# Optimization experiments

Measured on AMD Instinct MI355X. Metric: run time of the kernel, lower is better.

## Reference

```python
import jax, jax.numpy as jnp
import numpy as np

SEQ = 8192
DIM = 1280
NHEADS = 16
HEAD_DIM = DIM // NHEADS  # 80
NSEG = 8
SEG = SEQ // NSEG  # 1024


def setup_inputs() -> dict:
    key = jax.random.key(0)
    ks = jax.random.split(key, 7)
    hidden_states = jax.random.normal(ks[0], (SEQ, DIM), jnp.float32)
    # realistic rotary embeddings: cos/sin of random angles, shape [S, head_dim]
    ang = jax.random.uniform(ks[1], (SEQ, HEAD_DIM), jnp.float32, 0.0, 2.0 * np.pi)
    cos = jnp.cos(ang)
    sin = jnp.sin(ang)
    qkv_w = jax.random.normal(ks[2], (3 * DIM, DIM), jnp.float32) * (DIM ** -0.5)
    qkv_b = jax.random.normal(ks[3], (3 * DIM,), jnp.float32) * 0.02
    proj_w = jax.random.normal(ks[4], (DIM, DIM), jnp.float32) * (DIM ** -0.5)
    proj_b = jax.random.normal(ks[5], (DIM,), jnp.float32) * 0.02
    cu_seqlens = jnp.arange(NSEG + 1, dtype=jnp.int32) * SEG  # equal segments
    return {"hidden_states": hidden_states, "cos": cos, "sin": sin,
            "qkv_w": qkv_w, "qkv_b": qkv_b, "proj_w": proj_w, "proj_b": proj_b,
            "cu_seqlens": cu_seqlens}


def _rope(x, cos, sin):
    # x: [S, H, D]; cos/sin: [S, D] broadcast over heads. Computed in fp32.
    x = x.astype(jnp.float32)
    d = x.shape[-1]
    x1, x2 = x[..., : d // 2], x[..., d // 2:]
    rot = jnp.concatenate([-x2, x1], axis=-1)
    return x * cos[:, None, :] + rot * sin[:, None, :]


def reference(hidden_states, cos, sin, qkv_w, qkv_b, proj_w, proj_b, cu_seqlens):
    S, dim = hidden_states.shape
    nseg = cu_seqlens.shape[0] - 1
    seg = S // nseg  # segments are equal-length; block-diagonal attention batches over them
    H, D = NHEADS, dim // NHEADS

    qkv = hidden_states @ qkv_w.T + qkv_b                 # [S, 3*dim]
    qkv = qkv.reshape(S, 3, H, D)
    q, k, v = qkv[:, 0], qkv[:, 1], qkv[:, 2]             # [S, H, D]

    in_dtype = hidden_states.dtype
    q = _rope(q, cos, sin).astype(in_dtype)
    k = _rope(k, cos, sin).astype(in_dtype)

    scale = D ** -0.5
    qs = q.reshape(nseg, seg, H, D)
    ks = k.reshape(nseg, seg, H, D)
    vs = v.reshape(nseg, seg, H, D)

    scores = jnp.einsum('bqhd,bkhd->bhqk', qs, ks) * scale  # [nseg, H, seg, seg]
    probs = jax.nn.softmax(scores, axis=-1)
    out = jnp.einsum('bhqk,bkhd->bqhd', probs, vs)          # [nseg, seg, H, D]
    out = out.reshape(S, H * D)
    return out @ proj_w.T + proj_b
```

## Files before the change

kernel.cpp:

```cpp
#include <hip/hip_runtime.h>

#define SEQ 8192
#define DIM 1280
#define NHEADS 16
#define HD 80
#define HDP 96
#define NSEG 8
#define SEG 1024
#define KVB 64
#define NSTEP (SEG / KVB)
#define PST 72

typedef float f32x4 __attribute__((ext_vector_type(4)));
typedef short bf16x8 __attribute__((ext_vector_type(8)));
typedef unsigned int u32;

__device__ __forceinline__ float fast_exp2(float x) {
  return __builtin_amdgcn_exp2f(x);
}

__device__ __forceinline__ short f2bf(float f) {
  unsigned int u = __builtin_bit_cast(unsigned int, f);
  u = (u + 0x7fff + ((u >> 16) & 1)) >> 16;
  return (short)u;
}

__device__ __forceinline__ float bf2f(short s) {
  u32 u = ((u32)(unsigned short)s) << 16;
  return __builtin_bit_cast(float, u);
}

__device__ __forceinline__ u32 cvt_pk_bf16(float lo, float hi) {
  u32 r;
  asm("v_cvt_pk_bf16_f32 %0, %1, %2" : "=v"(r) : "v"(lo), "v"(hi));
  return r;
}

typedef __attribute__((address_space(1))) const unsigned int glds_src_t;
typedef __attribute__((address_space(3))) unsigned int glds_dst_t;
__device__ __forceinline__ void gload_lds16(const void* g, void* l) {
  __builtin_amdgcn_global_load_lds((glds_src_t*)g, (glds_dst_t*)l, 16, 0, 0);
}

__global__ void cast_f32_bf16(const float* __restrict__ in, short* __restrict__ out, int n) {
  int n4 = n >> 2;
  for (int i = blockIdx.x * blockDim.x + threadIdx.x; i < n4; i += gridDim.x * blockDim.x) {
    float4 v = ((const float4*)in)[i];
    short4 o;
    o.x = f2bf(v.x); o.y = f2bf(v.y); o.z = f2bf(v.z); o.w = f2bf(v.w);
    ((short4*)out)[i] = o;
  }
}

__global__ __launch_bounds__(512, 1) void gemm256(
    const short* __restrict__ A, const short* __restrict__ B,
    const float* __restrict__ bias, float* __restrict__ C,
    short* __restrict__ Cb, int M, int N, int K) {
  __shared__ short As[2][16384];
  __shared__ short Bs[2][16384];
  int tid = threadIdx.x;
  int w = tid >> 6, l = tid & 63;
  int lrow = l & 15, lg = l >> 4;
  int wm = w >> 2, wn = w & 3;
  int bid = blockIdx.x;
  int cpx = gridDim.x >> 3;
  int lid = (bid & 7) * cpx + (bid >> 3);
  int ntx = N >> 8;
  int m0 = (lid / ntx) * 256, n0 = (lid % ntx) * 256;

  const short* Ablk = A + (size_t)m0 * K;
  const short* Bblk = B + (size_t)n0 * K;

  f32x4 acc[8][4] = {};

#define STG_HALF(LDSB, GBASE, HALF, K0)                                       \
  {                                                                           \
    _Pragma("unroll") for (int rr = 0; rr < 2; rr++) {                        \
      int sb = rr * 512 + w * 64;                                             \
      int ss2 = sb + l;                                                       \
      int rl = ss2 >> 3, cc = ss2 & 7;                                        \
      int sl = cc ^ (rl & 7);                                                 \
      const short* sp = (GBASE) + (size_t)((HALF)*128 + rl) * K + (K0) + sl * 8; \
      gload_lds16(sp, (char*)(LDSB) + (HALF)*16384 + sb * 16);                \
    }                                                                         \
  }
#define LDA(MH, KS)                                                           \
  _Pragma("unroll") for (int mt = 0; mt < 4; mt++) {                          \
    int rowa = wm * 128 + ((MH)*4 + mt) * 16 + lrow;                          \
    int pa_ = ((KS)*4 + lg) ^ (rowa & 7);                                     \
    a[mt] = *(const bf16x8*)&As[cur][rowa * 64 + pa_ * 8];                    \
  }
#define LDB(KS)                                                               \
  _Pragma("unroll") for (int nt = 0; nt < 4; nt++) {                          \
    int rowb = wn * 64 + nt * 16 + lrow;                                      \
    int pb_ = ((KS)*4 + lg) ^ (rowb & 7);                                     \
    b[nt] = *(const bf16x8*)&Bs[cur][rowb * 64 + pb_ * 8];                    \
  }
#define MFMA16(MH)                                                            \
  _Pragma("unroll") for (int mt = 0; mt < 4; mt++)                            \
      _Pragma("unroll") for (int nt = 0; nt < 4; nt++)                        \
          acc[(MH)*4 + mt][nt] = __builtin_amdgcn_mfma_f32_16x16x32_bf16(     \
              a[mt], b[nt], acc[(MH)*4 + mt][nt], 0, 0, 0);

  {
    short* Ad = &As[0][0];
    short* Bd = &Bs[0][0];
    STG_HALF(Ad, Ablk, 0, 0);
    STG_HALF(Ad, Ablk, 1, 0);
    STG_HALF(Bd, Bblk, 0, 0);
    STG_HALF(Bd, Bblk, 1, 0);
  }
  asm volatile("s_waitcnt vmcnt(0)" ::: "memory");
  __builtin_amdgcn_s_barrier();
  asm volatile("" ::: "memory");

  int NT = K >> 6;
  for (int t = 0; t < NT; ++t) {
    int cur = t & 1;
    if (t + 1 < NT) {
      short* Ad = &As[cur ^ 1][0];
      short* Bd = &Bs[cur ^ 1][0];
      int k1 = (t + 1) << 6;
      STG_HALF(Ad, Ablk, 0, k1);
      STG_HALF(Ad, Ablk, 1, k1);
      STG_HALF(Bd, Bblk, 0, k1);
      STG_HALF(Bd, Bblk, 1, k1);
      asm volatile("s_waitcnt vmcnt(8)" ::: "memory");
    } else {
      asm volatile("s_waitcnt vmcnt(0)" ::: "memory");
    }
    __builtin_amdgcn_s_barrier();
    asm volatile("" ::: "memory");
    {
      bf16x8 a[4], b[4];
      __builtin_amdgcn_s_setprio(1);
      LDA(0, 0); LDB(0); MFMA16(0);
      LDA(1, 0); MFMA16(1);
      LDA(0, 1); LDB(1); MFMA16(0);
      LDA(1, 1); MFMA16(1);
      __builtin_amdgcn_s_setprio(0);
    }
    __builtin_amdgcn_s_barrier();
    asm volatile("" ::: "memory");
  }

  if (Cb) {
    short* E = &As[0][0];
#pragma unroll
    for (int s = 0; s < 4; s++) {
      __syncthreads();
      if (wm == (s >> 1)) {
#pragma unroll
        for (int mi = 0; mi < 4; mi++) {
          int mt2 = (s & 1) * 4 + mi;
#pragma unroll
          for (int nt = 0; nt < 4; nt++) {
            int col = wn * 64 + nt * 16 + lrow;
            float bv = bias[n0 + col];
#pragma unroll
            for (int r = 0; r < 4; r++)
              E[(mi * 16 + lg * 4 + r) * 264 + col] = f2bf(acc[mt2][nt][r] + bv);
          }
        }
      }
      __syncthreads();
#pragma unroll
      for (int j = 0; j < 4; j++) {
        int c = j * 512 + tid;
        int row = c >> 5, ch = c & 31;
        *(uint4*)&Cb[(size_t)(m0 + s * 64 + row) * N + n0 + ch * 8] =
            *(const uint4*)&E[row * 264 + ch * 8];
      }
    }
  } else {
#pragma unroll
    for (int nt = 0; nt < 4; nt++) {
      int col = n0 + wn * 64 + nt * 16 + lrow;
      float bv = bias[col];
#pragma unroll
      for (int mt = 0; mt < 8; mt++) {
        int mrow = m0 + wm * 128 + mt * 16 + lg * 4;
#pragma unroll
        for (int r = 0; r < 4; r++)
          C[(size_t)(mrow + r) * N + col] = acc[mt][nt][r] + bv;
      }
    }
  }
#undef STG_HALF
#undef LDA
#undef LDB
#undef MFMA16
}

__global__ __launch_bounds__(256) void gemm_bt_bias(
    const short* __restrict__ A, const short* __restrict__ B,
    const float* __restrict__ bias, float* __restrict__ C,
    short* __restrict__ Cb, int M, int N, int K) {
  __shared__ short As[2][128 * 64];
  __shared__ short Bs[2][128 * 64];
  int tid = threadIdx.x;
  int w = tid >> 6, l = tid & 63;
  int lrow = l & 15, lg = l >> 4;
  int bid = blockIdx.x;
  int cpx = gridDim.x >> 3;
  int lid = (bid & 7) * cpx + (bid >> 3);
  int ntx = N >> 7;
  int m0 = (lid / ntx) * 128, n0 = (lid % ntx) * 128;
  int wm = w & 1, wn = w >> 1;

  f32x4 acc[4][4] = {};

  const char* Abase = (const char*)A + (size_t)m0 * K * 2;
  const char* Bbase = (const char*)B + (size_t)n0 * K * 2;

#define STAGE_G(BUF, K0)                                                       \
  {                                                                            \
    _Pragma("unroll") for (int j = 0; j < 4; j++) {                            \
      int c = j * 256 + tid;                                                   \
      int row = c >> 3;                                                        \
      int slc = (c & 7) ^ (row & 7);                                           \
      size_t goff = (size_t)row * K * 2 + (size_t)(K0) * 2 + slc * 16;         \
      int loff = (j * 256 + w * 64) * 16;                                      \
      gload_lds16(Abase + goff, (char*)&As[BUF][0] + loff);                    \
      gload_lds16(Bbase + goff, (char*)&Bs[BUF][0] + loff);                    \
    }                                                                          \
  }

  STAGE_G(0, 0);
  asm volatile("s_waitcnt vmcnt(0)" ::: "memory");
  __builtin_amdgcn_s_barrier();
  asm volatile("" ::: "memory");

  for (int k0 = 0; k0 < K; k0 += 64) {
    int cur = (k0 >> 6) & 1;
    if (k0 + 64 < K) {
      STAGE_G(cur ^ 1, k0 + 64);
      asm volatile("s_waitcnt vmcnt(8)" ::: "memory");
    } else {
      asm volatile("s_waitcnt vmcnt(0)" ::: "memory");
    }
    __builtin_amdgcn_s_barrier();
    asm volatile("" ::: "memory");
#pragma unroll
    for (int kk = 0; kk < 2; kk++) {
      bf16x8 a[4], b[4];
#pragma unroll
      for (int mt = 0; mt < 4; mt++) {
        int row = wm * 64 + mt * 16 + lrow;
        int p = (kk * 4 + lg) ^ (row & 7);
        a[mt] = *(const bf16x8*)&As[cur][row * 64 + p * 8];
      }
#pragma unroll
      for (int nt = 0; nt < 4; nt++) {
        int row = wn * 64 + nt * 16 + lrow;
        int p = (kk * 4 + lg) ^ (row & 7);
        b[nt] = *(const bf16x8*)&Bs[cur][row * 64 + p * 8];
      }
#pragma unroll
      for (int mt = 0; mt < 4; mt++)
#pragma unroll
        for (int nt = 0; nt < 4; nt++)
          acc[mt][nt] = __builtin_amdgcn_mfma_f32_16x16x32_bf16(a[mt], b[nt], acc[mt][nt], 0, 0, 0);
    }
    __builtin_amdgcn_s_barrier();
    asm volatile("" ::: "memory");
  }

#pragma unroll
  for (int nt = 0; nt < 4; nt++) {
    int col = n0 + wn * 64 + nt * 16 + lrow;
    float bv = bias[col];
#pragma unroll
    for (int mt = 0; mt < 4; mt++) {
      int mrow = m0 + wm * 64 + mt * 16 + lg * 4;
      if (Cb) {
#pragma unroll
        for (int r = 0; r < 4; r++)
          Cb[(size_t)(mrow + r) * N + col] = f2bf(acc[mt][nt][r] + bv);
      } else {
#pragma unroll
        for (int r = 0; r < 4; r++)
          C[(size_t)(mrow + r) * N + col] = acc[mt][nt][r] + bv;
      }
    }
  }
}

__global__ void rope_qk(const short* __restrict__ qkv, const float* __restrict__ cosb,
                        const float* __restrict__ sinb, short* __restrict__ qg,
                        short* __restrict__ kg) {
  int t = blockIdx.x * blockDim.x + threadIdx.x;
  if (t >= SEQ * NHEADS * 40) return;
  int d = t % 40;
  int h = (t / 40) & 15;
  int s = t / 640;
  const short* row = qkv + (size_t)s * (3 * DIM);
  float c0 = cosb[s * HD + d], c1 = cosb[s * HD + d + 40];
  float s0 = sinb[s * HD + d], s1 = sinb[s * HD + d + 40];
  float x1 = bf2f(row[h * HD + d]), x2 = bf2f(row[h * HD + d + 40]);
  float q0 = x1 * c0 - x2 * s0;
  float q1 = x2 * c1 + x1 * s1;
  float y1 = bf2f(row[DIM + h * HD + d]), y2 = bf2f(row[DIM + h * HD + d + 40]);
  float k0 = y1 * c0 - y2 * s0;
  float k1 = y2 * c1 + y1 * s1;
  const float sc = 0.11180339887498949f * 1.4426950408889634f;
  size_t base = ((size_t)h * SEQ + s) * HDP;
  qg[base + d] = f2bf(q0 * sc);
  qg[base + d + 40] = f2bf(q1 * sc);
  kg[base + d] = f2bf(k0);
  kg[base + d + 40] = f2bf(k1);
  if (d < 16) { qg[base + 80 + d] = 0; kg[base + 80 + d] = 0; }
}

__global__ void v_transpose(const short* __restrict__ qkv, short* __restrict__ vt) {
  __shared__ short T[16][72];
  int st = blockIdx.x, dt = blockIdx.y, h = blockIdx.z;
  int d0 = dt * 16, s0 = st * 64;
  int t = threadIdx.x;
  int dd = t & 15, ss = t >> 4;
#pragma unroll
  for (int j = 0; j < 4; j++) {
    int s = ss + j * 16;
    T[dd][s] = qkv[(size_t)(s0 + s) * (3 * DIM) + 2 * DIM + h * HD + d0 + dd];
  }
  __syncthreads();
  int s2 = t & 63, dr = t >> 6;
#pragma unroll
  for (int j = 0; j < 4; j++) {
    int d = dr + j * 4;
    vt[((size_t)(h * HD + d0 + d)) * SEQ + s0 + s2] = T[d][s2];
  }
}

__global__ __launch_bounds__(256, 2) void attn_kernel(
    const short* __restrict__ qg, const short* __restrict__ kg,
    const short* __restrict__ vt, short* __restrict__ out) {
  __shared__ short Ks[2][64 * 128];
  __shared__ short Pl[4][32 * PST];
  int bid = blockIdx.x;
  int b = bid & 7, h = (bid >> 3) & 15, qt = bid >> 7;
  int tid = threadIdx.x;
  int w = tid >> 6, l = tid & 63;
  int lrow = l & 15, lg = l >> 4;
  int qbase_s = b * SEG + qt * 128 + w * 32;

  const short* qh = qg + (size_t)h * SEQ * HDP;
  const short* kh = kg + (size_t)h * SEQ * HDP;
  const short* vh = vt + (size_t)h * HD * SEQ;

#define STAGE_K(BUF, KEY0N)                                                    \
  {                                                                            \
    _Pragma("unroll") for (int sr = 0; sr < 4; sr++) {                         \
      int sbase = sr * 256 + w * 64;                                           \
      int ss = sbase + l;                                                      \
      int skey = ss >> 4, sc = ss & 15;                                        \
      int slc = sc ^ (skey & 7);                                               \
      const short* ssrc =                                                      \
          kh + (size_t)((KEY0N) + skey) * HDP + (slc < 12 ? slc * 8 : 0);      \
      gload_lds16(ssrc, (char*)&Ks[BUF][0] + sbase * 16);                      \
    }                                                                          \
  }

  bf16x8 qf[2][3];
#pragma unroll
  for (int mt = 0; mt < 2; mt++)
#pragma unroll
    for (int ks = 0; ks < 3; ks++)
      qf[mt][ks] = *(const bf16x8*)&qh[(size_t)(qbase_s + mt * 16 + lrow) * HDP + ks * 32 + lg * 8];

  f32x4 o[2][5] = {};
  float m_st[2] = {-1e30f, -1e30f};
  float l_st[2] = {0.f, 0.f};

  short* Pw = &Pl[w][0];

  STAGE_K(0, b * SEG);
  __syncthreads();

  for (int i = 0; i < NSTEP; i++) {
    int cur = i & 1;
    int key0 = b * SEG + i * KVB;
    if (i + 1 < NSTEP) {
      STAGE_K(cur ^ 1, key0 + KVB);
    }

    f32x4 sv[2][4] = {};
    __builtin_amdgcn_s_setprio(1);
#pragma unroll
    for (int kt = 0; kt < 4; kt++) {
      bf16x8 kf[3];
      int key = kt * 16 + lrow;
#pragma unroll
      for (int ks = 0; ks < 3; ks++) {
        int p = (ks * 4 + lg) ^ (key & 7);
        kf[ks] = *(const bf16x8*)&Ks[cur][key * 128 + p * 8];
      }
#pragma unroll
      for (int mt = 0; mt < 2; mt++)
#pragma unroll
        for (int ks = 0; ks < 3; ks++)
          sv[mt][kt] = __builtin_amdgcn_mfma_f32_16x16x32_bf16(kf[ks], qf[mt][ks], sv[mt][kt], 0, 0, 0);
    }
    __builtin_amdgcn_s_setprio(0);

    bf16x8 vf[5][2];
#pragma unroll
    for (int nt = 0; nt < 5; nt++)
#pragma unroll
      for (int ks = 0; ks < 2; ks++)
        vf[nt][ks] = *(const bf16x8*)&vh[(size_t)(nt * 16 + lrow) * SEQ + key0 + ks * 32 + lg * 8];

    float cm[2];
#pragma unroll
    for (int mt = 0; mt < 2; mt++) {
      float a0 = fmaxf(fmaxf(sv[mt][0][0], sv[mt][0][1]), fmaxf(sv[mt][0][2], sv[mt][0][3]));
      float a1 = fmaxf(fmaxf(sv[mt][1][0], sv[mt][1][1]), fmaxf(sv[mt][1][2], sv[mt][1][3]));
      float a2 = fmaxf(fmaxf(sv[mt][2][0], sv[mt][2][1]), fmaxf(sv[mt][2][2], sv[mt][2][3]));
      float a3 = fmaxf(fmaxf(sv[mt][3][0], sv[mt][3][1]), fmaxf(sv[mt][3][2], sv[mt][3][3]));
      float c = fmaxf(fmaxf(a0, a1), fmaxf(a2, a3));
      c = fmaxf(c, __shfl_xor(c, 16));
      c = fmaxf(c, __shfl_xor(c, 32));
      cm[mt] = c;
    }
    if (__any((cm[0] > m_st[0] + 8.f) || (cm[1] > m_st[1] + 8.f))) {
#pragma unroll
      for (int mt = 0; mt < 2; mt++) {
        float mn = fmaxf(m_st[mt], cm[mt]);
        float c = fast_exp2(m_st[mt] - mn);
        m_st[mt] = mn;
        l_st[mt] *= c;
        float cr[4];
#pragma unroll
        for (int r = 0; r < 4; r++) cr[r] = __shfl(c, lg * 4 + r);
#pragma unroll
        for (int nt = 0; nt < 5; nt++)
#pragma unroll
          for (int r = 0; r < 4; r++) o[mt][nt][r] *= cr[r];
      }
    }
#pragma unroll
    for (int mt = 0; mt < 2; mt++) {
      float rs = 0.f;
#pragma unroll
      for (int kt = 0; kt < 4; kt++) {
#pragma unroll
        for (int r = 0; r < 4; r++) {
          sv[mt][kt][r] = fast_exp2(sv[mt][kt][r] - m_st[mt]);
          rs += sv[mt][kt][r];
        }
        uint2 pk;
        pk.x = cvt_pk_bf16(sv[mt][kt][0], sv[mt][kt][1]);
        pk.y = cvt_pk_bf16(sv[mt][kt][2], sv[mt][kt][3]);
        *(uint2*)&Pw[(mt * 16 + lrow) * PST + kt * 16 + lg * 4] = pk;
      }
      rs += __shfl_xor(rs, 16);
      rs += __shfl_xor(rs, 32);
      l_st[mt] += rs;
    }

    bf16x8 pa[2][2];
#pragma unroll
    for (int mt = 0; mt < 2; mt++)
#pragma unroll
      for (int ks = 0; ks < 2; ks++)
        pa[mt][ks] = *(const bf16x8*)&Pw[(mt * 16 + lrow) * PST + ks * 32 + lg * 8];
    __builtin_amdgcn_s_setprio(1);
#pragma unroll
    for (int nt = 0; nt < 5; nt++)
#pragma unroll
      for (int mt = 0; mt < 2; mt++)
#pragma unroll
        for (int ks = 0; ks < 2; ks++)
          o[mt][nt] = __builtin_amdgcn_mfma_f32_16x16x32_bf16(pa[mt][ks], vf[nt][ks], o[mt][nt], 0, 0, 0);
    __builtin_amdgcn_s_setprio(0);

    __syncthreads();
  }

#pragma unroll
  for (int mt = 0; mt < 2; mt++) {
    float rl = 1.f / l_st[mt];
    float ir[4];
#pragma unroll
    for (int r = 0; r < 4; r++) ir[r] = __shfl(rl, lg * 4 + r);
#pragma unroll
    for (int r = 0; r < 4; r++) {
      int srow = qbase_s + mt * 16 + lg * 4 + r;
#pragma unroll
      for (int nt = 0; nt < 5; nt++)
        out[(size_t)srow * DIM + h * HD + nt * 16 + lrow] = f2bf(o[mt][nt][r] * ir[r]);
    }
  }
}

extern "C" void kernel_launch(void* const* d_in, const int* in_sizes, int n_in,
                              void* d_out, int out_size, void* d_ws, size_t ws_size,
                              hipStream_t stream) {
  const float* hidden = (const float*)d_in[0];
  const float* cosb = (const float*)d_in[1];
  const float* sinb = (const float*)d_in[2];
  const float* qkv_w = (const float*)d_in[3];
  const float* qkv_b = (const float*)d_in[4];
  const float* proj_w = (const float*)d_in[5];
  const float* proj_b = (const float*)d_in[6];

  char* ws = (char*)d_ws;
  short* qkv_bf = (short*)(ws);
  short* attn_o = (short*)(ws);
  short* wp_bf = (short*)(ws + 23068672);
  short* q_bf = (short*)(ws + 125829120);
  short* k_bf = (short*)(ws + 150994944);
  short* v_tb = (short*)(ws + 176160768);
  short* h_bf = (short*)(ws + 197132288);
  short* wq_bf = (short*)(ws + 218103808);

  cast_f32_bf16<<<4096, 256, 0, stream>>>(hidden, h_bf, SEQ * DIM);
  cast_f32_bf16<<<4096, 256, 0, stream>>>(qkv_w, wq_bf, 3 * DIM * DIM);
  gemm256<<<480, 512, 0, stream>>>(h_bf, wq_bf, qkv_b, nullptr, qkv_bf, SEQ, 3 * DIM, DIM);
  rope_qk<<<20480, 256, 0, stream>>>(qkv_bf, cosb, sinb, q_bf, k_bf);
  v_transpose<<<dim3(128, 5, 16), 256, 0, stream>>>(qkv_bf, v_tb);
  cast_f32_bf16<<<2048, 256, 0, stream>>>(proj_w, wp_bf, DIM * DIM);
  attn_kernel<<<1024, 256, 0, stream>>>(q_bf, k_bf, v_tb, attn_o);
  gemm_bt_bias<<<640, 256, 0, stream>>>(attn_o, wp_bf, proj_b, (float*)d_out, nullptr, SEQ, DIM, DIM);
}
```

Baseline: 308.4 us.

## Halve gemm256 K-tile to 32 to fit two blocks per CU

Shrinks the 256x256 GEMM's K-step from 64 to 32, cutting shared memory from 128KB to 64KB. The LDS swizzle and staging are reworked for the narrower 32-element rows, and launch bounds are raised to allow two 512-thread blocks per CU. The goal is higher occupancy so one block's global loads can overlap the other's MFMA work. In exchange there are twice as many barriers and pipeline steps per K. Register pressure from the 128 accumulator floats under the two-block bound may cause spills.

```diff
diff --git a/kernel.cpp b/kernel.cpp
--- a/kernel.cpp
+++ b/kernel.cpp
@@ -52,12 +52,11 @@
   }
 }
 
-__global__ __launch_bounds__(512, 1) void gemm256(
+__global__ __launch_bounds__(512, 2) void gemm256(
     const short* __restrict__ A, const short* __restrict__ B,
     const float* __restrict__ bias, float* __restrict__ C,
     short* __restrict__ Cb, int M, int N, int K) {
-  __shared__ short As[2][16384];
-  __shared__ short Bs[2][16384];
+  __shared__ short Sh[32768];
   int tid = threadIdx.x;
   int w = tid >> 6, l = tid & 63;
   int lrow = l & 15, lg = l >> 4;
@@ -73,59 +72,49 @@
 
   f32x4 acc[8][4] = {};
 
-#define STG_HALF(LDSB, GBASE, HALF, K0)                                       \
+#define STG32(BUF, OPB, GBASE, K0)                                            \
   {                                                                           \
     _Pragma("unroll") for (int rr = 0; rr < 2; rr++) {                        \
       int sb = rr * 512 + w * 64;                                             \
       int ss2 = sb + l;                                                       \
-      int rl = ss2 >> 3, cc = ss2 & 7;                                        \
-      int sl = cc ^ (rl & 7);                                                 \
-      const short* sp = (GBASE) + (size_t)((HALF)*128 + rl) * K + (K0) + sl * 8; \
-      gload_lds16(sp, (char*)(LDSB) + (HALF)*16384 + sb * 16);                \
+      int rl = ss2 >> 2, cc = ss2 & 3;                                        \
+      int sl = cc ^ ((rl >> 1) & 3);                                          \
+      const short* sp = (GBASE) + (size_t)rl * K + (K0) + sl * 8;             \
+      gload_lds16(sp, (char*)Sh + (OPB)*32768 + (BUF)*16384 + sb * 16);       \
     }                                                                         \
   }
-#define LDA(MH, KS)                                                           \
+#define LDA32(MH)                                                             \
   _Pragma("unroll") for (int mt = 0; mt < 4; mt++) {                          \
     int rowa = wm * 128 + ((MH)*4 + mt) * 16 + lrow;                          \
-    int pa_ = ((KS)*4 + lg) ^ (rowa & 7);                                     \
-    a[mt] = *(const bf16x8*)&As[cur][rowa * 64 + pa_ * 8];                    \
-  }
-#define LDB(KS)                                                               \
+    int pa_ = lg ^ ((rowa >> 1) & 3);                                         \
+    a[mt] = *(const bf16x8*)&Sh[cur * 8192 + rowa * 32 + pa_ * 8];            \
+  }
+#define LDB32()                                                               \
   _Pragma("unroll") for (int nt = 0; nt < 4; nt++) {                          \
     int rowb = wn * 64 + nt * 16 + lrow;                                      \
-    int pb_ = ((KS)*4 + lg) ^ (rowb & 7);                                     \
-    b[nt] = *(const bf16x8*)&Bs[cur][rowb * 64 + pb_ * 8];                    \
-  }
-#define MFMA16(MH)                                                            \
+    int pb_ = lg ^ ((rowb >> 1) & 3);                                         \
+    b[nt] = *(const bf16x8*)&Sh[16384 + cur * 8192 + rowb * 32 + pb_ * 8];    \
+  }
+#define MFMA16X(MH)                                                           \
   _Pragma("unroll") for (int mt = 0; mt < 4; mt++)                            \
       _Pragma("unroll") for (int nt = 0; nt < 4; nt++)                        \
           acc[(MH)*4 + mt][nt] = __builtin_amdgcn_mfma_f32_16x16x32_bf16(     \
               a[mt], b[nt], acc[(MH)*4 + mt][nt], 0, 0, 0);
 
-  {
-    short* Ad = &As[0][0];
-    short* Bd = &Bs[0][0];
-    STG_HALF(Ad, Ablk, 0, 0);
-    STG_HALF(Ad, Ablk, 1, 0);
-    STG_HALF(Bd, Bblk, 0, 0);
-    STG_HALF(Bd, Bblk, 1, 0);
-  }
+  STG32(0, 0, Ablk, 0);
+  STG32(0, 1, Bblk, 0);
   asm volatile("s_waitcnt vmcnt(0)" ::: "memory");
   __builtin_amdgcn_s_barrier();
   asm volatile("" ::: "memory");
 
-  int NT = K >> 6;
+  int NT = K >> 5;
   for (int t = 0; t < NT; ++t) {
     int cur = t & 1;
     if (t + 1 < NT) {
-      short* Ad = &As[cur ^ 1][0];
-      short* Bd = &Bs[cur ^ 1][0];
-      int k1 = (t + 1) << 6;
-      STG_HALF(Ad, Ablk, 0, k1);
-      STG_HALF(Ad, Ablk, 1, k1);
-      STG_HALF(Bd, Bblk, 0, k1);
-      STG_HALF(Bd, Bblk, 1, k1);
-      asm volatile("s_waitcnt vmcnt(8)" ::: "memory");
+      int k1 = (t + 1) << 5;
+      STG32(cur ^ 1, 0, Ablk, k1);
+      STG32(cur ^ 1, 1, Bblk, k1);
+      asm volatile("s_waitcnt vmcnt(4)" ::: "memory");
     } else {
       asm volatile("s_waitcnt vmcnt(0)" ::: "memory");
     }
@@ -134,10 +123,8 @@
     {
       bf16x8 a[4], b[4];
       __builtin_amdgcn_s_setprio(1);
-      LDA(0, 0); LDB(0); MFMA16(0);
-      LDA(1, 0); MFMA16(1);
-      LDA(0, 1); LDB(1); MFMA16(0);
-      LDA(1, 1); MFMA16(1);
+      LDA32(0); LDB32(); MFMA16X(0);
+      LDA32(1); MFMA16X(1);
       __builtin_amdgcn_s_setprio(0);
     }
     __builtin_amdgcn_s_barrier();
@@ -145,7 +132,6 @@
   }
 
   if (Cb) {
-    short* E = &As[0][0];
 #pragma unroll
     for (int s = 0; s < 4; s++) {
       __syncthreads();
@@ -159,7 +145,7 @@
             float bv = bias[n0 + col];
 #pragma unroll
             for (int r = 0; r < 4; r++)
-              E[(mi * 16 + lg * 4 + r) * 264 + col] = f2bf(acc[mt2][nt][r] + bv);
+              Sh[(mi * 16 + lg * 4 + r) * 264 + col] = f2bf(acc[mt2][nt][r] + bv);
           }
         }
       }
@@ -169,7 +155,7 @@
         int c = j * 512 + tid;
         int row = c >> 5, ch = c & 31;
         *(uint4*)&Cb[(size_t)(m0 + s * 64 + row) * N + n0 + ch * 8] =
-            *(const uint4*)&E[row * 264 + ch * 8];
+            *(const uint4*)&Sh[row * 264 + ch * 8];
       }
     }
   } else {
@@ -186,10 +172,10 @@
       }
     }
   }
-#undef STG_HALF
-#undef LDA
-#undef LDB
-#undef MFMA16
+#undef STG32
+#undef LDA32
+#undef LDB32
+#undef MFMA16X
 }
 
 __global__ __launch_bounds__(256) void gemm_bt_bias(
```

New measurement: 301.3 us. -2.3%, faster.
